# Performance work log

Hardware: AMD Instinct MI355X
Metric: run time of the kernel (lower is better)

Reference implementation:

```python
import jax, jax.numpy as jnp
import numpy as np

B, N, E, DIN, DOUT = 2, 50000, 800000, 128, 128
ALPHA = 0.2  # LeakyReLU negative slope


def setup_inputs() -> dict:
    key = jax.random.key(0)
    k1, k2, k3, k4 = jax.random.split(key, 4)
    h = jax.random.normal(k1, (B, N, DIN), dtype=jnp.float32)
    edge_index = jax.random.randint(k4, (2, E), 0, N, dtype=jnp.int32)
    # Linear(in, out, bias=False): weight shape [out, in]
    W_fc = jax.random.normal(k2, (DOUT, DIN), dtype=jnp.float32) / np.sqrt(DIN)
    # Linear(2*out, 1, bias=False): weight shape [1, 2*out]
    W_attn = jax.random.normal(k3, (1, 2 * DOUT), dtype=jnp.float32) / np.sqrt(2 * DOUT)
    return {"h": h, "edge_index": edge_index, "W_fc": W_fc, "W_attn": W_attn}


def reference(h, edge_index, W_fc, W_attn):
    # Wh: [B, N, DOUT]
    Wh = jnp.einsum("bni,oi->bno", h, W_fc)
    src, dst = edge_index[0], edge_index[1]
    # attn_fc([src_h, dst_h]) == src_h @ a_src + dst_h @ a_dst
    a = W_attn[0]
    a_src, a_dst = a[:DOUT], a[DOUT:]
    s_src = Wh @ a_src  # [B, N]
    s_dst = Wh @ a_dst  # [B, N]
    e = jax.nn.leaky_relu(s_src[:, src] + s_dst[:, dst], ALPHA)  # [B, E]
    # segment softmax over destination groups (segment ops need leading E axis)
    eT = e.T  # [E, B]
    m = jax.ops.segment_max(eT, dst, num_segments=N)  # [N, B]; -inf for empty segs (never gathered)
    ex = jnp.exp(eT - m[dst])  # [E, B]
    denom = jax.ops.segment_sum(ex, dst, num_segments=N)  # [N, B]
    attn = ex / denom[dst]  # [E, B]
    # weighted scatter-add of source features: msg [E, B, DOUT]
    msg = attn[:, :, None] * jnp.transpose(Wh, (1, 0, 2))[src]
    out = jax.ops.segment_sum(msg, dst, num_segments=N)  # [N, B, DOUT]
    return jax.nn.elu(jnp.transpose(out, (1, 0, 2)))  # [B, N, DOUT]
```

## Files before the change

### kernel.cpp

```cpp
#include <hip/hip_runtime.h>
#include <math.h>

#define NN 50000
#define EE 800000
#define DDIM 128
#define NROWS 100000
#define NBIN 391
#define NCHUNK 391

typedef __attribute__((ext_vector_type(8))) short bf16x8;
typedef __attribute__((ext_vector_type(4))) float f32x4;

__device__ __forceinline__ float lrelu(float x) { return x > 0.f ? x : 0.2f * x; }
__device__ __forceinline__ float eluf(float x)  {
    float e = __expf(x);
    return x > 0.f ? x : e - 1.f;
}

__device__ __forceinline__ unsigned short f2bf(float f) {
    unsigned int u = __float_as_uint(f);
    u += 0x7fffu + ((u >> 16) & 1u);
    return (unsigned short)(u >> 16);
}
__device__ __forceinline__ float bflo(unsigned int v) { return __uint_as_float(v << 16); }
__device__ __forceinline__ float bfhi(unsigned int v) { return __uint_as_float(v & 0xffff0000u); }

__global__ __launch_bounds__(256) void histW_kernel(const int* __restrict__ ei,
                                                    int* __restrict__ histmat,
                                                    const float* __restrict__ Wfc,
                                                    unsigned short* __restrict__ Wsw) {
    const int tid = threadIdx.x;
    if (blockIdx.x < NCHUNK) {
        __shared__ int lcnt[NBIN];
        for (int i = tid; i < NBIN; i += 256) lcnt[i] = 0;
        __syncthreads();
        const int cbase = blockIdx.x * 2048;
        const int cnt   = min(2048, EE - cbase);
#pragma unroll
        for (int r = 0; r < 8; ++r) {
            int el = r * 256 + tid;
            if (el < cnt) {
                int dst = ei[EE + cbase + el];
                atomicAdd(&lcnt[dst >> 7], 1);
            }
        }
        __syncthreads();
        for (int i = tid; i < NBIN; i += 256)
            histmat[blockIdx.x * NBIN + i] = lcnt[i];
        return;
    }
    const int col = tid & 127;
    const int kh  = tid >> 7;
#pragma unroll
    for (int q8 = 0; q8 < 8; ++q8) {
        int k0 = kh * 64 + q8 * 8;
        float4 w0 = *(const float4*)&Wfc[col * DDIM + k0];
        float4 w1 = *(const float4*)&Wfc[col * DDIM + k0 + 4];
        union { uint4 q4; unsigned short u[8]; } pk;
        pk.u[0] = f2bf(w0.x); pk.u[1] = f2bf(w0.y);
        pk.u[2] = f2bf(w0.z); pk.u[3] = f2bf(w0.w);
        pk.u[4] = f2bf(w1.x); pk.u[5] = f2bf(w1.y);
        pk.u[6] = f2bf(w1.z); pk.u[7] = f2bf(w1.w);
        int chunk = (k0 >> 3) ^ (col & 15);
        *(uint4*)((char*)Wsw + col * 256 + chunk * 16) = pk.q4;
    }
}

__global__ __launch_bounds__(64) void colscan_kernel(const int* __restrict__ histmat,
                                                     int* __restrict__ chunkstart,
                                                     int* __restrict__ bintot) {
    const int bin  = blockIdx.x;
    const int lane = threadIdx.x;
    int carry = 0;
#pragma unroll
    for (int it = 0; it < 7; ++it) {
        int c = it * 64 + lane;
        int v = (c < NCHUNK) ? histmat[c * NBIN + bin] : 0;
        int x = v;
#pragma unroll
        for (int o = 1; o < 64; o <<= 1) {
            int t = __shfl_up(x, o);
            if (lane >= o) x += t;
        }
        if (c < NCHUNK) chunkstart[bin * NCHUNK + c] = carry + x - v;
        carry += __shfl(x, 63);
    }
    if (lane == 0) bintot[bin] = carry;
}

__global__ __launch_bounds__(64) void binscan_kernel(const int* __restrict__ bintot,
                                                     int* __restrict__ binbase) {
    const int lane = threadIdx.x;
    int carry = 0;
#pragma unroll
    for (int it = 0; it < 7; ++it) {
        int c = it * 64 + lane;
        int v = (c < NBIN) ? bintot[c] : 0;
        int x = v;
#pragma unroll
        for (int o = 1; o < 64; o <<= 1) {
            int t = __shfl_up(x, o);
            if (lane >= o) x += t;
        }
        if (c < NBIN) binbase[c] = carry + x - v;
        carry += __shfl(x, 63);
    }
    if (lane == 0) binbase[NBIN] = carry;
}

__global__ __launch_bounds__(256) void gemm_kernel(const float* __restrict__ h,
                                                   const unsigned short* __restrict__ Wsw,
                                                   const float* __restrict__ Wat,
                                                   unsigned short* __restrict__ Wh16,
                                                   float* __restrict__ ssrc,
                                                   float* __restrict__ sdst) {
    __shared__ unsigned int Wlds_u32[8192];
    __shared__ unsigned short stage[64 * 136];
    char* WldsB  = (char*)Wlds_u32;
    char* stageB = (char*)stage;
    const int tid  = threadIdx.x;
    const int lane = tid & 63;
    const int wv   = tid >> 6;

    {
        const char* gsrc = (const char*)Wsw + wv * 8192 + lane * 16;
        unsigned int* ldst = &Wlds_u32[wv * 2048];
#pragma unroll
        for (int c8 = 0; c8 < 8; ++c8) {
            __builtin_amdgcn_global_load_lds((const unsigned int*)(gsrc + c8 * 1024),
                                             ldst + c8 * 256, 16, 0, 0);
        }
    }

    const long mbase  = (long)blockIdx.x * 64 + wv * 16;
    const bool active = (mbase < NROWS);
    const long mload  = active ? mbase : 0;
    const int c  = lane & 15;
    const int kg = lane >> 4;

    union Af { bf16x8 v; unsigned short u[8]; };
    Af af[4];
    const float* arow = h + (mload + c) * DDIM + kg * 8;
#pragma unroll
    for (int kk = 0; kk < 4; ++kk) {
        float4 x = *(const float4*)(arow + kk * 32);
        float4 y = *(const float4*)(arow + kk * 32 + 4);
        af[kk].u[0] = f2bf(x.x); af[kk].u[1] = f2bf(x.y);
        af[kk].u[2] = f2bf(x.z); af[kk].u[3] = f2bf(x.w);
        af[kk].u[4] = f2bf(y.x); af[kk].u[5] = f2bf(y.y);
        af[kk].u[6] = f2bf(y.z); af[kk].u[7] = f2bf(y.w);
    }
    __syncthreads();
    if (!active) return;

    f32x4 acc[8];
#pragma unroll
    for (int t = 0; t < 8; ++t) acc[t] = (f32x4){0.f, 0.f, 0.f, 0.f};
#pragma unroll
    for (int t = 0; t < 8; ++t) {
        int colbase = (t * 16 + c) * 256;
        int sw = c << 4;
#pragma unroll
        for (int kk = 0; kk < 4; ++kk) {
            int ba = (colbase + kk * 64 + kg * 16) ^ sw;
            bf16x8 b = *(const bf16x8*)(WldsB + ba);
            acc[t] = __builtin_amdgcn_mfma_f32_16x16x32_bf16(af[kk].v, b, acc[t], 0, 0, 0);
        }
    }

#pragma unroll
    for (int t = 0; t < 8; ++t) {
#pragma unroll
        for (int r = 0; r < 4; ++r) {
            int lrow = wv * 16 + kg * 4 + r;
            *(unsigned short*)(stageB + lrow * 272 + (t * 16 + c) * 2) = f2bf(acc[t][r]);
        }
    }
    {
        const long gbase = mbase * 256;
        const int  lbase = wv * 16 * 272;
#pragma unroll
        for (int q = 0; q < 4; ++q) {
            int f = q * 1024 + lane * 16;
            uint4 v = *(const uint4*)(stageB + lbase + (f >> 8) * 272 + (f & 255));
            *(uint4*)((char*)Wh16 + gbase + f) = v;
        }
    }

    float asv[8], adv[8];
#pragma unroll
    for (int t = 0; t < 8; ++t) {
        asv[t] = Wat[t * 16 + c];
        adv[t] = Wat[DDIM + t * 16 + c];
    }
#pragma unroll
    for (int r = 0; r < 4; ++r) {
        float ps = 0.f, pd = 0.f;
#pragma unroll
        for (int t = 0; t < 8; ++t) {
            ps += acc[t][r] * asv[t];
            pd += acc[t][r] * adv[t];
        }
#pragma unroll
        for (int o = 1; o <= 8; o <<= 1) {
            ps += __shfl_xor(ps, o);
            pd += __shfl_xor(pd, o);
        }
        if (c == 0) {
            long row = mbase + kg * 4 + r;
            ssrc[row] = ps;
            sdst[row] = pd;
        }
    }
}

__global__ __launch_bounds__(256) void scatterA_kernel(const int* __restrict__ ei,
                                                       const int* __restrict__ binbase,
                                                       const int* __restrict__ chunkstart,
                                                       unsigned int* __restrict__ records) {
    __shared__ int lcnt[NBIN];
    const int tid = threadIdx.x;
    for (int i = tid; i < NBIN; i += 256) lcnt[i] = 0;
    __syncthreads();
    const int cb  = blockIdx.x * 2048;
    const int cnt = min(2048, EE - cb);
#pragma unroll
    for (int r = 0; r < 8; ++r) {
        int el = r * 256 + tid;
        if (el < cnt) {
            int e   = cb + el;
            int dst = ei[EE + e];
            int src = ei[e];
            int bin = dst >> 7;
            int rank = atomicAdd(&lcnt[bin], 1);
            int pos = binbase[bin] + chunkstart[bin * NCHUNK + blockIdx.x] + rank;
            records[pos] = (unsigned)src | ((unsigned)(dst & 127) << 16);
        }
    }
}

__global__ __launch_bounds__(256) void scatterB_kernel(const unsigned int* __restrict__ records,
                                                       const int* __restrict__ binbase,
                                                       int* __restrict__ offs,
                                                       int* __restrict__ slist) {
    __shared__ int cnt[128];
    __shared__ int cbase[128];
    const int b = blockIdx.x, tid = threadIdx.x;
    const int start = binbase[b];
    const int end   = binbase[b + 1];
    const int span  = end - start;

    if (tid < 128) cnt[tid] = 0;
    __syncthreads();
    for (int i = tid; i < span; i += 256)
        atomicAdd(&cnt[records[start + i] >> 16], 1);
    __syncthreads();
    if (tid < 64) {
        int l = tid;
        int c0 = cnt[l], c1 = cnt[64 + l];
        int s0 = c0, s1 = c1;
#pragma unroll
        for (int o = 1; o < 64; o <<= 1) { int t = __shfl_up(s0, o); if (l >= o) s0 += t; }
        int t0 = __shfl(s0, 63);
#pragma unroll
        for (int o = 1; o < 64; o <<= 1) { int t = __shfl_up(s1, o); if (l >= o) s1 += t; }
        cbase[l]      = s0 - c0;
        cbase[64 + l] = t0 + s1 - c1;
    }
    __syncthreads();
    if (tid < 128) {
        offs[b * 128 + tid] = start + cbase[tid];
        cnt[tid] = 0;
    }
    __syncthreads();
    for (int i = tid; i < span; i += 256) {
        unsigned int r = records[start + i];
        int dl = (int)(r >> 16);
        int pos = atomicAdd(&cnt[dl], 1);
        slist[start + cbase[dl] + pos] = (int)(r & 0xFFFFu);
    }
}

__global__ __launch_bounds__(256) void aggregate_kernel(const unsigned int* __restrict__ Wh16u,
                                                        const int* __restrict__ offs,
                                                        const int* __restrict__ slist,
                                                        const float* __restrict__ ssrc,
                                                        const float* __restrict__ sdst,
                                                        float* __restrict__ out) {
    const int lane = threadIdx.x & 63;
    const int wid  = threadIdx.x >> 6;
    const int bid  = blockIdx.x;
    const int b    = bid & 1;
    const int d    = (bid >> 1) * 4 + wid;

    const int grp = lane >> 4;
    const int fl  = lane & 15;

    float* o = out + ((long)b * NN + d) * DDIM;

    const int base   = offs[d];
    const int degree = offs[d + 1] - base;
    if (degree == 0) {
        if (lane < 16) {
            float4 z = {0.f, 0.f, 0.f, 0.f};
            ((float4*)o)[2 * fl]     = z;
            ((float4*)o)[2 * fl + 1] = z;
        }
        return;
    }

    const long boff = (long)b * NN;
    const float sdv = sdst[boff + d];
    const float* ssb = ssrc + boff;
    const unsigned int* WB = Wh16u + boff * 64;

    f32x4 accA = {0,0,0,0}, accB = {0,0,0,0};
    float ds = 0.f;

    for (int ch = 0; ch < degree; ch += 64) {
        int i = ch + lane;
        int s = 0; float w = 0.f;
        if (i < degree) {
            s = slist[base + i];
            w = __expf(lrelu(ssb[s] + sdv));
            ds += w;
        }
        int cnt   = min(64, degree - ch);
        int quads = (cnt + 3) >> 2;
        for (int j = 0; j < quads; ++j) {
            int idx = 4 * j + grp;
            int   sj = __shfl(s, idx);
            float wj = __shfl(w, idx);
            uint4 v = ((const uint4*)(WB + (long)sj * 64))[fl];
            accA.x += wj * bflo(v.x); accA.y += wj * bfhi(v.x);
            accA.z += wj * bflo(v.y); accA.w += wj * bfhi(v.y);
            accB.x += wj * bflo(v.z); accB.y += wj * bfhi(v.z);
            accB.z += wj * bflo(v.w); accB.w += wj * bfhi(v.w);
        }
    }

#pragma unroll
    for (int m = 32; m >= 16; m >>= 1) {
        accA.x += __shfl_xor(accA.x, m); accA.y += __shfl_xor(accA.y, m);
        accA.z += __shfl_xor(accA.z, m); accA.w += __shfl_xor(accA.w, m);
        accB.x += __shfl_xor(accB.x, m); accB.y += __shfl_xor(accB.y, m);
        accB.z += __shfl_xor(accB.z, m); accB.w += __shfl_xor(accB.w, m);
    }
#pragma unroll
    for (int m = 32; m > 0; m >>= 1) ds += __shfl_xor(ds, m);
    const float inv = 1.f / ds;

    if (lane < 16) {
        float4 rA = { eluf(accA.x * inv), eluf(accA.y * inv),
                      eluf(accA.z * inv), eluf(accA.w * inv) };
        float4 rB = { eluf(accB.x * inv), eluf(accB.y * inv),
                      eluf(accB.z * inv), eluf(accB.w * inv) };
        ((float4*)o)[2 * fl]     = rA;
        ((float4*)o)[2 * fl + 1] = rB;
    }
}

extern "C" void kernel_launch(void* const* d_in, const int* in_sizes, int n_in,
                              void* d_out, int out_size, void* d_ws, size_t ws_size,
                              hipStream_t stream) {
    (void)in_sizes; (void)n_in; (void)out_size; (void)ws_size;
    const float* h   = (const float*)d_in[0];
    const int*   ei  = (const int*)d_in[1];
    const float* Wfc = (const float*)d_in[2];
    const float* Wat = (const float*)d_in[3];
    float* out = (float*)d_out;

    char* ws = (char*)d_ws;
    unsigned short* Wh16 = (unsigned short*)(ws + 0);
    float*  ssrc  = (float*)(ws + 25600000);
    float*  sdst  = (float*)(ws + 26000000);
    int*    slist = (int*)  (ws + 26400000);
    unsigned int* records = (unsigned int*)(ws + 29600000);
    int*    offs      = (int*)(ws + 32800000);
    int*    histmat   = (int*)(ws + 33000192);
    int*    chunkstart= (int*)(ws + 33611716);
    int*    bintot    = (int*)(ws + 34223240);
    int*    binbase   = (int*)(ws + 34224804);
    unsigned short* Wsw = (unsigned short*)(ws + 34226384);

    histW_kernel<<<NCHUNK + 1, 256, 0, stream>>>(ei, histmat, Wfc, Wsw);
    colscan_kernel<<<NBIN, 64, 0, stream>>>(histmat, chunkstart, bintot);
    binscan_kernel<<<1, 64, 0, stream>>>(bintot, binbase);
    gemm_kernel<<<(NROWS + 63) / 64, 256, 0, stream>>>(h, Wsw, Wat, Wh16, ssrc, sdst);
    scatterA_kernel<<<NCHUNK, 256, 0, stream>>>(ei, binbase, chunkstart, records);
    scatterB_kernel<<<NBIN, 256, 0, stream>>>(records, binbase, offs, slist);
    aggregate_kernel<<<25000, 256, 0, stream>>>((const unsigned int*)Wh16, offs,
                                                slist, ssrc, sdst, out);
}
```

Before: 118.9 us.

## Fuse histogram into GEMM launch and split aggregate feature halves across blocks

The destination histogram blocks now run inside the GEMM kernel's grid, as a separate block range, so the histogram and the projection GEMM run concurrently. W preparation moves to a tiny separate launch ahead of them. The aggregate kernel now handles half of the feature dimension per block, with 8 lanes per edge and two destinations per wave. This reads more edges in parallel per wave, but the softmax weights are recomputed twice per edge, once for each half.

Measured after the change: 144.6 us. 21.7% more time.

```diff
diff --git a/kernel.cpp b/kernel.cpp
--- a/kernel.cpp
+++ b/kernel.cpp
@@ -7,6 +7,7 @@
 #define NROWS 100000
 #define NBIN 391
 #define NCHUNK 391
+#define GEMMB 1563
 
 typedef __attribute__((ext_vector_type(8))) short bf16x8;
 typedef __attribute__((ext_vector_type(4))) float f32x4;
@@ -25,30 +26,9 @@
 __device__ __forceinline__ float bflo(unsigned int v) { return __uint_as_float(v << 16); }
 __device__ __forceinline__ float bfhi(unsigned int v) { return __uint_as_float(v & 0xffff0000u); }
 
-__global__ __launch_bounds__(256) void histW_kernel(const int* __restrict__ ei,
-                                                    int* __restrict__ histmat,
-                                                    const float* __restrict__ Wfc,
+__global__ __launch_bounds__(256) void wprep_kernel(const float* __restrict__ Wfc,
                                                     unsigned short* __restrict__ Wsw) {
     const int tid = threadIdx.x;
-    if (blockIdx.x < NCHUNK) {
-        __shared__ int lcnt[NBIN];
-        for (int i = tid; i < NBIN; i += 256) lcnt[i] = 0;
-        __syncthreads();
-        const int cbase = blockIdx.x * 2048;
-        const int cnt   = min(2048, EE - cbase);
-#pragma unroll
-        for (int r = 0; r < 8; ++r) {
-            int el = r * 256 + tid;
-            if (el < cnt) {
-                int dst = ei[EE + cbase + el];
-                atomicAdd(&lcnt[dst >> 7], 1);
-            }
-        }
-        __syncthreads();
-        for (int i = tid; i < NBIN; i += 256)
-            histmat[blockIdx.x * NBIN + i] = lcnt[i];
-        return;
-    }
     const int col = tid & 127;
     const int kh  = tid >> 7;
 #pragma unroll
@@ -66,59 +46,38 @@
     }
 }
 
-__global__ __launch_bounds__(64) void colscan_kernel(const int* __restrict__ histmat,
-                                                     int* __restrict__ chunkstart,
-                                                     int* __restrict__ bintot) {
-    const int bin  = blockIdx.x;
-    const int lane = threadIdx.x;
-    int carry = 0;
-#pragma unroll
-    for (int it = 0; it < 7; ++it) {
-        int c = it * 64 + lane;
-        int v = (c < NCHUNK) ? histmat[c * NBIN + bin] : 0;
-        int x = v;
-#pragma unroll
-        for (int o = 1; o < 64; o <<= 1) {
-            int t = __shfl_up(x, o);
-            if (lane >= o) x += t;
-        }
-        if (c < NCHUNK) chunkstart[bin * NCHUNK + c] = carry + x - v;
-        carry += __shfl(x, 63);
-    }
-    if (lane == 0) bintot[bin] = carry;
-}
-
-__global__ __launch_bounds__(64) void binscan_kernel(const int* __restrict__ bintot,
-                                                     int* __restrict__ binbase) {
-    const int lane = threadIdx.x;
-    int carry = 0;
-#pragma unroll
-    for (int it = 0; it < 7; ++it) {
-        int c = it * 64 + lane;
-        int v = (c < NBIN) ? bintot[c] : 0;
-        int x = v;
-#pragma unroll
-        for (int o = 1; o < 64; o <<= 1) {
-            int t = __shfl_up(x, o);
-            if (lane >= o) x += t;
-        }
-        if (c < NBIN) binbase[c] = carry + x - v;
-        carry += __shfl(x, 63);
-    }
-    if (lane == 0) binbase[NBIN] = carry;
-}
-
-__global__ __launch_bounds__(256) void gemm_kernel(const float* __restrict__ h,
-                                                   const unsigned short* __restrict__ Wsw,
-                                                   const float* __restrict__ Wat,
-                                                   unsigned short* __restrict__ Wh16,
-                                                   float* __restrict__ ssrc,
-                                                   float* __restrict__ sdst) {
+__global__ __launch_bounds__(256) void fused_kernel(const int* __restrict__ ei,
+                                                    int* __restrict__ histmat,
+                                                    const float* __restrict__ h,
+                                                    const unsigned short* __restrict__ Wsw,
+                                                    const float* __restrict__ Wat,
+                                                    unsigned short* __restrict__ Wh16,
+                                                    float* __restrict__ ssrc,
+                                                    float* __restrict__ sdst) {
     __shared__ unsigned int Wlds_u32[8192];
     __shared__ unsigned short stage[64 * 136];
+    const int tid = threadIdx.x;
+
+    if (blockIdx.x < NCHUNK) {
+        int* lcnt = (int*)Wlds_u32;
+        for (int i = tid; i < NBIN; i += 256) lcnt[i] = 0;
+        __syncthreads();
+        const int cb  = blockIdx.x * 2048;
+        const int cnt = min(2048, EE - cb);
+#pragma unroll
+        for (int r = 0; r < 8; ++r) {
+            int el = r * 256 + tid;
+            if (el < cnt) atomicAdd(&lcnt[ei[EE + cb + el] >> 7], 1);
+        }
+        __syncthreads();
+        for (int i = tid; i < NBIN; i += 256)
+            histmat[blockIdx.x * NBIN + i] = lcnt[i];
+        return;
+    }
+
     char* WldsB  = (char*)Wlds_u32;
     char* stageB = (char*)stage;
-    const int tid  = threadIdx.x;
+    const int gb   = blockIdx.x - NCHUNK;
     const int lane = tid & 63;
     const int wv   = tid >> 6;
 
@@ -132,7 +91,7 @@
         }
     }
 
-    const long mbase  = (long)blockIdx.x * 64 + wv * 16;
+    const long mbase  = (long)gb * 64 + wv * 16;
     const bool active = (mbase < NROWS);
     const long mload  = active ? mbase : 0;
     const int c  = lane & 15;
@@ -212,6 +171,48 @@
             sdst[row] = pd;
         }
     }
+}
+
+__global__ __launch_bounds__(64) void colscan_kernel(const int* __restrict__ histmat,
+                                                     int* __restrict__ chunkstart,
+                                                     int* __restrict__ bintot) {
+    const int bin  = blockIdx.x;
+    const int lane = threadIdx.x;
+    int carry = 0;
+#pragma unroll
+    for (int it = 0; it < 7; ++it) {
+        int c = it * 64 + lane;
+        int v = (c < NCHUNK) ? histmat[c * NBIN + bin] : 0;
+        int x = v;
+#pragma unroll
+        for (int o = 1; o < 64; o <<= 1) {
+            int t = __shfl_up(x, o);
+            if (lane >= o) x += t;
+        }
+        if (c < NCHUNK) chunkstart[bin * NCHUNK + c] = carry + x - v;
+        carry += __shfl(x, 63);
+    }
+    if (lane == 0) bintot[bin] = carry;
+}
+
+__global__ __launch_bounds__(64) void binscan_kernel(const int* __restrict__ bintot,
+                                                     int* __restrict__ binbase) {
+    const int lane = threadIdx.x;
+    int carry = 0;
+#pragma unroll
+    for (int it = 0; it < 7; ++it) {
+        int c = it * 64 + lane;
+        int v = (c < NBIN) ? bintot[c] : 0;
+        int x = v;
+#pragma unroll
+        for (int o = 1; o < 64; o <<= 1) {
+            int t = __shfl_up(x, o);
+            if (lane >= o) x += t;
+        }
+        if (c < NBIN) binbase[c] = carry + x - v;
+        carry += __shfl(x, 63);
+    }
+    if (lane == 0) binbase[NBIN] = carry;
 }
 
 __global__ __launch_bounds__(256) void scatterA_kernel(const int* __restrict__ ei,
@@ -290,73 +291,76 @@
     const int lane = threadIdx.x & 63;
     const int wid  = threadIdx.x >> 6;
     const int bid  = blockIdx.x;
-    const int b    = bid & 1;
-    const int d    = (bid >> 1) * 4 + wid;
-
-    const int grp = lane >> 4;
-    const int fl  = lane & 15;
-
-    float* o = out + ((long)b * NN + d) * DDIM;
-
-    const int base   = offs[d];
-    const int degree = offs[d + 1] - base;
-    if (degree == 0) {
-        if (lane < 16) {
-            float4 z = {0.f, 0.f, 0.f, 0.f};
-            ((float4*)o)[2 * fl]     = z;
-            ((float4*)o)[2 * fl + 1] = z;
-        }
-        return;
-    }
-
+    const int cmb  = bid & 3;
+    const int b    = cmb >> 1;
+    const int half = cmb & 1;
+    const int d2   = (bid >> 2) * 4 + wid;
+
+    const int grp = lane >> 3;
+    const int fl  = lane & 7;
     const long boff = (long)b * NN;
-    const float sdv = sdst[boff + d];
     const float* ssb = ssrc + boff;
-    const unsigned int* WB = Wh16u + boff * 64;
-
-    f32x4 accA = {0,0,0,0}, accB = {0,0,0,0};
-    float ds = 0.f;
-
-    for (int ch = 0; ch < degree; ch += 64) {
-        int i = ch + lane;
-        int s = 0; float w = 0.f;
-        if (i < degree) {
-            s = slist[base + i];
-            w = __expf(lrelu(ssb[s] + sdv));
-            ds += w;
-        }
-        int cnt   = min(64, degree - ch);
-        int quads = (cnt + 3) >> 2;
-        for (int j = 0; j < quads; ++j) {
-            int idx = 4 * j + grp;
-            int   sj = __shfl(s, idx);
-            float wj = __shfl(w, idx);
-            uint4 v = ((const uint4*)(WB + (long)sj * 64))[fl];
-            accA.x += wj * bflo(v.x); accA.y += wj * bfhi(v.x);
-            accA.z += wj * bflo(v.y); accA.w += wj * bfhi(v.y);
-            accB.x += wj * bflo(v.z); accB.y += wj * bfhi(v.z);
-            accB.z += wj * bflo(v.w); accB.w += wj * bfhi(v.w);
-        }
-    }
-
-#pragma unroll
-    for (int m = 32; m >= 16; m >>= 1) {
-        accA.x += __shfl_xor(accA.x, m); accA.y += __shfl_xor(accA.y, m);
-        accA.z += __shfl_xor(accA.z, m); accA.w += __shfl_xor(accA.w, m);
-        accB.x += __shfl_xor(accB.x, m); accB.y += __shfl_xor(accB.y, m);
-        accB.z += __shfl_xor(accB.z, m); accB.w += __shfl_xor(accB.w, m);
-    }
-#pragma unroll
-    for (int m = 32; m > 0; m >>= 1) ds += __shfl_xor(ds, m);
-    const float inv = 1.f / ds;
-
-    if (lane < 16) {
-        float4 rA = { eluf(accA.x * inv), eluf(accA.y * inv),
-                      eluf(accA.z * inv), eluf(accA.w * inv) };
-        float4 rB = { eluf(accB.x * inv), eluf(accB.y * inv),
-                      eluf(accB.z * inv), eluf(accB.w * inv) };
-        ((float4*)o)[2 * fl]     = rA;
-        ((float4*)o)[2 * fl + 1] = rB;
+    const unsigned int* WBh = Wh16u + boff * 64 + half * 32;
+
+#pragma unroll
+    for (int dd = 0; dd < 2; ++dd) {
+        const int d = d2 * 2 + dd;
+        float* o = out + (boff + d) * DDIM + half * 64;
+        const int base   = offs[d];
+        const int degree = offs[d + 1] - base;
+        if (degree == 0) {
+            if (lane < 8) {
+                float4 z = {0.f, 0.f, 0.f, 0.f};
+                ((float4*)o)[2 * fl]     = z;
+                ((float4*)o)[2 * fl + 1] = z;
+            }
+            continue;
+        }
+        const float sdv = sdst[boff + d];
+        f32x4 accA = {0,0,0,0}, accB = {0,0,0,0};
+        float ds = 0.f;
+
+        for (int ch = 0; ch < degree; ch += 64) {
+            int i = ch + lane;
+            int s = 0; float w = 0.f;
+            if (i < degree) {
+                s = slist[base + i];
+                w = __expf(lrelu(ssb[s] + sdv));
+                ds += w;
+            }
+            int cnt = min(64, degree - ch);
+            int qn  = (cnt + 7) >> 3;
+            for (int j = 0; j < qn; ++j) {
+                int idx = 8 * j + grp;
+                int   sj = __shfl(s, idx);
+                float wj = __shfl(w, idx);
+                uint4 v = ((const uint4*)(WBh + (long)sj * 64))[fl];
+                accA.x += wj * bflo(v.x); accA.y += wj * bfhi(v.x);
+                accA.z += wj * bflo(v.y); accA.w += wj * bfhi(v.y);
+                accB.x += wj * bflo(v.z); accB.y += wj * bfhi(v.z);
+                accB.z += wj * bflo(v.w); accB.w += wj * bfhi(v.w);
+            }
+        }
+
+#pragma unroll
+        for (int m = 32; m >= 8; m >>= 1) {
+            accA.x += __shfl_xor(accA.x, m); accA.y += __shfl_xor(accA.y, m);
+            accA.z += __shfl_xor(accA.z, m); accA.w += __shfl_xor(accA.w, m);
+            accB.x += __shfl_xor(accB.x, m); accB.y += __shfl_xor(accB.y, m);
+            accB.z += __shfl_xor(accB.z, m); accB.w += __shfl_xor(accB.w, m);
+        }
+#pragma unroll
+        for (int m = 32; m > 0; m >>= 1) ds += __shfl_xor(ds, m);
+        const float inv = 1.f / ds;
+
+        if (lane < 8) {
+            float4 rA = { eluf(accA.x * inv), eluf(accA.y * inv),
+                          eluf(accA.z * inv), eluf(accA.w * inv) };
+            float4 rB = { eluf(accB.x * inv), eluf(accB.y * inv),
+                          eluf(accB.z * inv), eluf(accB.w * inv) };
+            ((float4*)o)[2 * fl]     = rA;
+            ((float4*)o)[2 * fl + 1] = rB;
+        }
     }
 }
 
@@ -383,10 +387,11 @@
     int*    binbase   = (int*)(ws + 34224804);
     unsigned short* Wsw = (unsigned short*)(ws + 34226384);
 
-    histW_kernel<<<NCHUNK + 1, 256, 0, stream>>>(ei, histmat, Wfc, Wsw);
+    wprep_kernel<<<1, 256, 0, stream>>>(Wfc, Wsw);
+    fused_kernel<<<NCHUNK + GEMMB, 256, 0, stream>>>(ei, histmat, h, Wsw, Wat,
+                                                     Wh16, ssrc, sdst);
     colscan_kernel<<<NBIN, 64, 0, stream>>>(histmat, chunkstart, bintot);
     binscan_kernel<<<1, 64, 0, stream>>>(bintot, binbase);
-    gemm_kernel<<<(NROWS + 63) / 64, 256, 0, stream>>>(h, Wsw, Wat, Wh16, ssrc, sdst);
     scatterA_kernel<<<NCHUNK, 256, 0, stream>>>(ei, binbase, chunkstart, records);
     scatterB_kernel<<<NBIN, 256, 0, stream>>>(records, binbase, offs, slist);
     aggregate_kernel<<<25000, 256, 0, stream>>>((const unsigned int*)Wh16, offs,
```

## Fuse edge histogram into GEMM launch and precompute per-bin bases in scatterA

Applied to the files above, without the earlier changes.

The destination histogram blocks and the GEMM blocks now run as one launch, split by block index, so the histogram work overlaps with the GEMM. The W bf16 swizzle prep moves to its own tiny preceding kernel. scatterA now computes each bin's base offset once into shared memory instead of reading two global arrays per edge. The fused launch uses the GEMM's large LDS footprint for the histogram blocks too, and it adds a small separate launch.

New measurement: 116.5 us. 2.0% less time.

```diff
diff --git a/kernel.cpp b/kernel.cpp
--- a/kernel.cpp
+++ b/kernel.cpp
@@ -7,6 +7,7 @@
 #define NROWS 100000
 #define NBIN 391
 #define NCHUNK 391
+#define GEMMB 1563
 
 typedef __attribute__((ext_vector_type(8))) short bf16x8;
 typedef __attribute__((ext_vector_type(4))) float f32x4;
@@ -25,30 +26,9 @@
 __device__ __forceinline__ float bflo(unsigned int v) { return __uint_as_float(v << 16); }
 __device__ __forceinline__ float bfhi(unsigned int v) { return __uint_as_float(v & 0xffff0000u); }
 
-__global__ __launch_bounds__(256) void histW_kernel(const int* __restrict__ ei,
-                                                    int* __restrict__ histmat,
-                                                    const float* __restrict__ Wfc,
+__global__ __launch_bounds__(256) void wprep_kernel(const float* __restrict__ Wfc,
                                                     unsigned short* __restrict__ Wsw) {
     const int tid = threadIdx.x;
-    if (blockIdx.x < NCHUNK) {
-        __shared__ int lcnt[NBIN];
-        for (int i = tid; i < NBIN; i += 256) lcnt[i] = 0;
-        __syncthreads();
-        const int cbase = blockIdx.x * 2048;
-        const int cnt   = min(2048, EE - cbase);
-#pragma unroll
-        for (int r = 0; r < 8; ++r) {
-            int el = r * 256 + tid;
-            if (el < cnt) {
-                int dst = ei[EE + cbase + el];
-                atomicAdd(&lcnt[dst >> 7], 1);
-            }
-        }
-        __syncthreads();
-        for (int i = tid; i < NBIN; i += 256)
-            histmat[blockIdx.x * NBIN + i] = lcnt[i];
-        return;
-    }
     const int col = tid & 127;
     const int kh  = tid >> 7;
 #pragma unroll
@@ -66,59 +46,38 @@
     }
 }
 
-__global__ __launch_bounds__(64) void colscan_kernel(const int* __restrict__ histmat,
-                                                     int* __restrict__ chunkstart,
-                                                     int* __restrict__ bintot) {
-    const int bin  = blockIdx.x;
-    const int lane = threadIdx.x;
-    int carry = 0;
-#pragma unroll
-    for (int it = 0; it < 7; ++it) {
-        int c = it * 64 + lane;
-        int v = (c < NCHUNK) ? histmat[c * NBIN + bin] : 0;
-        int x = v;
-#pragma unroll
-        for (int o = 1; o < 64; o <<= 1) {
-            int t = __shfl_up(x, o);
-            if (lane >= o) x += t;
-        }
-        if (c < NCHUNK) chunkstart[bin * NCHUNK + c] = carry + x - v;
-        carry += __shfl(x, 63);
-    }
-    if (lane == 0) bintot[bin] = carry;
-}
-
-__global__ __launch_bounds__(64) void binscan_kernel(const int* __restrict__ bintot,
-                                                     int* __restrict__ binbase) {
-    const int lane = threadIdx.x;
-    int carry = 0;
-#pragma unroll
-    for (int it = 0; it < 7; ++it) {
-        int c = it * 64 + lane;
-        int v = (c < NBIN) ? bintot[c] : 0;
-        int x = v;
-#pragma unroll
-        for (int o = 1; o < 64; o <<= 1) {
-            int t = __shfl_up(x, o);
-            if (lane >= o) x += t;
-        }
-        if (c < NBIN) binbase[c] = carry + x - v;
-        carry += __shfl(x, 63);
-    }
-    if (lane == 0) binbase[NBIN] = carry;
-}
-
-__global__ __launch_bounds__(256) void gemm_kernel(const float* __restrict__ h,
-                                                   const unsigned short* __restrict__ Wsw,
-                                                   const float* __restrict__ Wat,
-                                                   unsigned short* __restrict__ Wh16,
-                                                   float* __restrict__ ssrc,
-                                                   float* __restrict__ sdst) {
+__global__ __launch_bounds__(256) void fused_kernel(const int* __restrict__ ei,
+                                                    int* __restrict__ histmat,
+                                                    const float* __restrict__ h,
+                                                    const unsigned short* __restrict__ Wsw,
+                                                    const float* __restrict__ Wat,
+                                                    unsigned short* __restrict__ Wh16,
+                                                    float* __restrict__ ssrc,
+                                                    float* __restrict__ sdst) {
     __shared__ unsigned int Wlds_u32[8192];
     __shared__ unsigned short stage[64 * 136];
+    const int tid = threadIdx.x;
+
+    if (blockIdx.x < NCHUNK) {
+        int* lcnt = (int*)Wlds_u32;
+        for (int i = tid; i < NBIN; i += 256) lcnt[i] = 0;
+        __syncthreads();
+        const int cb  = blockIdx.x * 2048;
+        const int cnt = min(2048, EE - cb);
+#pragma unroll
+        for (int r = 0; r < 8; ++r) {
+            int el = r * 256 + tid;
+            if (el < cnt) atomicAdd(&lcnt[ei[EE + cb + el] >> 7], 1);
+        }
+        __syncthreads();
+        for (int i = tid; i < NBIN; i += 256)
+            histmat[blockIdx.x * NBIN + i] = lcnt[i];
+        return;
+    }
+
     char* WldsB  = (char*)Wlds_u32;
     char* stageB = (char*)stage;
-    const int tid  = threadIdx.x;
+    const int gb   = blockIdx.x - NCHUNK;
     const int lane = tid & 63;
     const int wv   = tid >> 6;
 
@@ -132,7 +91,7 @@
         }
     }
 
-    const long mbase  = (long)blockIdx.x * 64 + wv * 16;
+    const long mbase  = (long)gb * 64 + wv * 16;
     const bool active = (mbase < NROWS);
     const long mload  = active ? mbase : 0;
     const int c  = lane & 15;
@@ -214,13 +173,59 @@
     }
 }
 
+__global__ __launch_bounds__(64) void colscan_kernel(const int* __restrict__ histmat,
+                                                     int* __restrict__ chunkstart,
+                                                     int* __restrict__ bintot) {
+    const int bin  = blockIdx.x;
+    const int lane = threadIdx.x;
+    int carry = 0;
+#pragma unroll
+    for (int it = 0; it < 7; ++it) {
+        int c = it * 64 + lane;
+        int v = (c < NCHUNK) ? histmat[c * NBIN + bin] : 0;
+        int x = v;
+#pragma unroll
+        for (int o = 1; o < 64; o <<= 1) {
+            int t = __shfl_up(x, o);
+            if (lane >= o) x += t;
+        }
+        if (c < NCHUNK) chunkstart[bin * NCHUNK + c] = carry + x - v;
+        carry += __shfl(x, 63);
+    }
+    if (lane == 0) bintot[bin] = carry;
+}
+
+__global__ __launch_bounds__(64) void binscan_kernel(const int* __restrict__ bintot,
+                                                     int* __restrict__ binbase) {
+    const int lane = threadIdx.x;
+    int carry = 0;
+#pragma unroll
+    for (int it = 0; it < 7; ++it) {
+        int c = it * 64 + lane;
+        int v = (c < NBIN) ? bintot[c] : 0;
+        int x = v;
+#pragma unroll
+        for (int o = 1; o < 64; o <<= 1) {
+            int t = __shfl_up(x, o);
+            if (lane >= o) x += t;
+        }
+        if (c < NBIN) binbase[c] = carry + x - v;
+        carry += __shfl(x, 63);
+    }
+    if (lane == 0) binbase[NBIN] = carry;
+}
+
 __global__ __launch_bounds__(256) void scatterA_kernel(const int* __restrict__ ei,
                                                        const int* __restrict__ binbase,
                                                        const int* __restrict__ chunkstart,
                                                        unsigned int* __restrict__ records) {
     __shared__ int lcnt[NBIN];
+    __shared__ int lbase[NBIN];
     const int tid = threadIdx.x;
-    for (int i = tid; i < NBIN; i += 256) lcnt[i] = 0;
+    for (int i = tid; i < NBIN; i += 256) {
+        lcnt[i]  = 0;
+        lbase[i] = binbase[i] + chunkstart[i * NCHUNK + blockIdx.x];
+    }
     __syncthreads();
     const int cb  = blockIdx.x * 2048;
     const int cnt = min(2048, EE - cb);
@@ -233,8 +238,7 @@
             int src = ei[e];
             int bin = dst >> 7;
             int rank = atomicAdd(&lcnt[bin], 1);
-            int pos = binbase[bin] + chunkstart[bin * NCHUNK + blockIdx.x] + rank;
-            records[pos] = (unsigned)src | ((unsigned)(dst & 127) << 16);
+            records[lbase[bin] + rank] = (unsigned)src | ((unsigned)(dst & 127) << 16);
         }
     }
 }
@@ -383,10 +387,11 @@
     int*    binbase   = (int*)(ws + 34224804);
     unsigned short* Wsw = (unsigned short*)(ws + 34226384);
 
-    histW_kernel<<<NCHUNK + 1, 256, 0, stream>>>(ei, histmat, Wfc, Wsw);
+    wprep_kernel<<<1, 256, 0, stream>>>(Wfc, Wsw);
+    fused_kernel<<<NCHUNK + GEMMB, 256, 0, stream>>>(ei, histmat, h, Wsw, Wat,
+                                                     Wh16, ssrc, sdst);
     colscan_kernel<<<NBIN, 64, 0, stream>>>(histmat, chunkstart, bintot);
     binscan_kernel<<<1, 64, 0, stream>>>(bintot, binbase);
-    gemm_kernel<<<(NROWS + 63) / 64, 256, 0, stream>>>(h, Wsw, Wat, Wh16, ssrc, sdst);
     scatterA_kernel<<<NCHUNK, 256, 0, stream>>>(ei, binbase, chunkstart, records);
     scatterB_kernel<<<NBIN, 256, 0, stream>>>(records, binbase, offs, slist);
     aggregate_kernel<<<25000, 256, 0, stream>>>((const unsigned int*)Wh16, offs,
```
